# Kernel tuning notes

Measured on AMD Instinct MI355X. Metric: run time of the kernel, lower is better.

The kernel has to match this reference:

```python
import jax, jax.numpy as jnp
import numpy as np

B_CHUNK = 5          # hardcoded self.B in the module
GAMMA = 0.9865
BATCH, SEQ, FEAT, DIM = 8, 4000, 256, 256


def setup_inputs() -> dict:
    key = jax.random.key(0)
    ks = jax.random.split(key, 6)
    xq = jax.random.normal(ks[0], (BATCH, SEQ, FEAT), jnp.float32)
    xk = jax.random.normal(ks[1], (BATCH, SEQ, FEAT), jnp.float32)
    xv = jax.random.normal(ks[2], (BATCH, SEQ, FEAT), jnp.float32)
    scale = 1.0 / np.sqrt(FEAT).astype(np.float32)
    Wq = jax.random.normal(ks[3], (FEAT, DIM), jnp.float32) * scale
    Wk = jax.random.normal(ks[4], (FEAT, DIM), jnp.float32) * scale
    Wv = jax.random.normal(ks[5], (FEAT, DIM), jnp.float32) * scale
    return {"xq": xq, "xk": xk, "xv": xv, "Wq": Wq, "Wk": Wk, "Wv": Wv}


def reference(xq, xk, xv, Wq, Wk, Wv):
    gamma = jnp.float32(GAMMA)
    B = B_CHUNK
    b, seq, _ = xq.shape
    dim = Wq.shape[1]
    n = seq // B  # number of chunks

    # projections, chunked: [b, n, B, dim]
    Q = (xq @ Wq).reshape(b, n, B, dim)
    K = (xk @ Wk).reshape(b, n, B, dim)
    V = (xv @ Wv).reshape(b, n, B, dim)

    chunk_idx = jnp.arange(n, dtype=jnp.float32)
    # Z[i] = gamma^(B - i - 1) (per-chunk scalar, as in original)
    Z = gamma ** (jnp.float32(B) - chunk_idx - 1.0)
    Vz = V * Z[None, :, None, None]

    # intra-chunk decay matrix: L[i,j] = gamma^(j-i) for i >= j, else 0
    pos = jnp.arange(B, dtype=jnp.float32)
    L = jnp.tril(gamma ** (pos[None, :] - pos[:, None]))

    # intra-chunk term: (Q K^T * L) @ V, vectorized over all chunks
    S = jnp.einsum('bnid,bnjd->bnij', Q, K)          # [b, n, B, B]
    intra = jnp.einsum('bnij,bnjd->bnid', S * L, V)  # [b, n, B, dim]

    # cross-chunk recurrence: R[i] = K_i^T Vz_i + gamma^B R[i-1]
    # X[i-1] += Q_i @ R[i-1] * gamma^(i+1)
    Qn = jnp.moveaxis(Q, 1, 0)   # [n, b, B, dim]
    Kn = jnp.moveaxis(K, 1, 0)
    Vzn = jnp.moveaxis(Vz, 1, 0)
    gB = gamma ** B

    def step(R_prev, inp):
        qi, ki, vzi, i = inp
        cross_prev = jnp.einsum('bod,bde->boe', qi, R_prev) * gamma ** (i + 1.0)
        R_new = jnp.einsum('bod,boe->bde', ki, vzi) + gB * R_prev
        return R_new, cross_prev

    R0 = jnp.zeros((b, dim, dim), xq.dtype)
    _, ys = jax.lax.scan(step, R0, (Qn, Kn, Vzn, chunk_idx))  # ys[i] = cross for chunk i-1
    cross = jnp.concatenate([ys[1:], jnp.zeros_like(ys[:1])], axis=0)  # last chunk has no cross term
    cross = jnp.moveaxis(cross, 0, 1)  # [b, n, B, dim]

    X = intra + cross
    return X.reshape(b, seq, dim)
```

## Files before the change

kernel.cpp:

```cpp
#include <hip/hip_runtime.h>
#include <cmath>

#define GAMMA 0.9865f
#define L2G   -0.01960905f
#define BATCH 8
#define SEQ   4000
#define CSUP  25
#define GSUP  32
#define RPG   125

typedef _Float16 half8 __attribute__((ext_vector_type(8)));
typedef _Float16 half4 __attribute__((ext_vector_type(4)));
typedef float    floatx4 __attribute__((ext_vector_type(4)));

__device__ __forceinline__ float gpow(float e) { return exp2f(e * L2G); }

__global__ __launch_bounds__(256) void wt_convert(
    const float* __restrict__ Wq, const float* __restrict__ Wk, const float* __restrict__ Wv,
    _Float16* __restrict__ Wt) {
    int t = blockIdx.x * 256 + threadIdx.x;
    int mat = t >> 16, rem = t & 65535;
    int n = rem >> 8, k = rem & 255;
    const float* W = (mat == 0) ? Wq : (mat == 1) ? Wk : Wv;
    Wt[(size_t)mat * 65536 + n * 256 + k] = (_Float16)W[k * 256 + n];
}

__global__ __launch_bounds__(256, 2) void qkv_gemm_f16(
    const float* __restrict__ xq, const float* __restrict__ xk, const float* __restrict__ xv,
    const _Float16* __restrict__ WtAll,
    _Float16* __restrict__ Qb, _Float16* __restrict__ Kb, _Float16* __restrict__ Vb) {
    int op = blockIdx.y;
    const float* x = (op == 0) ? xq : (op == 1) ? xk : xv;
    const _Float16* Wt = WtAll + (size_t)op * 65536;
    _Float16* dst = (op == 0) ? Qb : (op == 1) ? Kb : Vb;

    __shared__ _Float16 Xs[128][40];
    __shared__ _Float16 WsT[256][40];

    int t = threadIdx.x;
    int lane = t & 63, wave = t >> 6;
    int ln = lane & 15, q8 = (lane >> 4) << 3, q4 = (lane >> 4) << 2;
    int row0 = blockIdx.x * 128;

    floatx4 acc[8][4] = {};

    for (int dt = 0; dt < 8; ++dt) {
        int k0 = dt * 32;
#pragma unroll
        for (int i = 0; i < 4; ++i) {
            int idx = t + i * 256;
            int m = idx >> 3, kk = (idx & 7) << 2;
            floatx4 v = *(const floatx4*)&x[(size_t)(row0 + m) * 256 + k0 + kk];
            half4 h; h[0] = (_Float16)v[0]; h[1] = (_Float16)v[1];
            h[2] = (_Float16)v[2]; h[3] = (_Float16)v[3];
            *(half4*)&Xs[m][kk] = h;
        }
#pragma unroll
        for (int i = 0; i < 4; ++i) {
            int idx = t + i * 256;
            int n = idx >> 2, kk = (idx & 3) << 3;
            *(half8*)&WsT[n][kk] = *(const half8*)&Wt[n * 256 + k0 + kk];
        }
        __syncthreads();
        half8 af[8];
#pragma unroll
        for (int mi = 0; mi < 8; ++mi) af[mi] = *(const half8*)&Xs[mi * 16 + ln][q8];
#pragma unroll
        for (int ni = 0; ni < 4; ++ni) {
            half8 bf = *(const half8*)&WsT[(wave * 4 + ni) * 16 + ln][q8];
#pragma unroll
            for (int mi = 0; mi < 8; ++mi)
                acc[mi][ni] = __builtin_amdgcn_mfma_f32_16x16x32_f16(af[mi], bf, acc[mi][ni], 0, 0, 0);
        }
        __syncthreads();
    }
#pragma unroll
    for (int mi = 0; mi < 8; ++mi)
#pragma unroll
        for (int ni = 0; ni < 4; ++ni)
#pragma unroll
            for (int r = 0; r < 4; ++r) {
                int row = row0 + mi * 16 + q4 + r;
                int col = (wave * 4 + ni) * 16 + ln;
                dst[(size_t)row * 256 + col] = (_Float16)acc[mi][ni][r];
            }
}

__global__ __launch_bounds__(256, 2) void chunk_states_mfma(
    const _Float16* __restrict__ Kb, const _Float16* __restrict__ Vb,
    _Float16* __restrict__ Wh) {
    int eh = blockIdx.x, g = blockIdx.y, b = blockIdx.z;
    int t = threadIdx.x, lane = t & 63, wave = t >> 6;
    int ln = lane & 15, q8 = (lane >> 4) << 3, q4 = (lane >> 4) << 2;
    __shared__ __align__(16) _Float16 Vs[32 * 136];
    __shared__ __align__(16) _Float16 Ks[32 * 264];
    size_t base_row = (size_t)b * SEQ + g * RPG;
    floatx4 acc[8][4] = {};
    for (int kt = 0; kt < 4; ++kt) {
        int r0 = kt * 32;
#pragma unroll
        for (int i = 0; i < 2; ++i) {
            int idx = t + i * 256;
            int r = idx >> 4, e8 = (idx & 15) << 3;
            half8 v = {};
            if (r0 + r < RPG) {
                v = *(const half8*)&Vb[(base_row + r0 + r) * 256 + eh * 128 + e8];
                int mloc = (r0 + r) / 5;
                float a = gpow((float)(149 - 6 * mloc));
#pragma unroll
                for (int z = 0; z < 8; ++z) v[z] = (_Float16)((float)v[z] * a);
            }
            *(half8*)&Vs[r * 136 + e8] = v;
        }
#pragma unroll
        for (int i = 0; i < 4; ++i) {
            int idx = t + i * 256;
            int r = idx >> 5, d8 = (idx & 31) << 3;
            half8 v = {};
            if (r0 + r < RPG) v = *(const half8*)&Kb[(base_row + r0 + r) * 256 + d8];
            *(half8*)&Ks[r * 264 + d8] = v;
        }
        __syncthreads();
        half8 Af[8], Bf[4];
#pragma unroll
        for (int mi = 0; mi < 8; ++mi)
#pragma unroll
            for (int j = 0; j < 8; ++j) Af[mi][j] = Vs[(q8 + j) * 136 + mi * 16 + ln];
#pragma unroll
        for (int ni = 0; ni < 4; ++ni)
#pragma unroll
            for (int j = 0; j < 8; ++j) Bf[ni][j] = Ks[(q8 + j) * 264 + wave * 64 + ni * 16 + ln];
#pragma unroll
        for (int mi = 0; mi < 8; ++mi)
#pragma unroll
            for (int ni = 0; ni < 4; ++ni)
                acc[mi][ni] = __builtin_amdgcn_mfma_f32_16x16x32_f16(Af[mi], Bf[ni], acc[mi][ni], 0, 0, 0);
        __syncthreads();
    }
    size_t ob = ((size_t)(g * 8 + b)) << 16;
#pragma unroll
    for (int mi = 0; mi < 8; ++mi)
#pragma unroll
        for (int ni = 0; ni < 4; ++ni)
#pragma unroll
            for (int r = 0; r < 4; ++r) {
                int e = eh * 128 + mi * 16 + q4 + r;
                int d = wave * 64 + ni * 16 + ln;
                Wh[ob + (size_t)e * 256 + d] = (_Float16)acc[mi][ni][r];
            }
}

__global__ __launch_bounds__(256) void state_scan(
    const _Float16* __restrict__ Wh, _Float16* __restrict__ SprevT) {
    int t = blockIdx.x * 256 + threadIdx.x;
    int b = t >> 13;
    int idx = (t & 8191) << 3;
    const float gF = gpow(150.0f);
    float s[8] = {};
    for (int g = 0; g < GSUP; ++g) {
        size_t o = (((size_t)(g * 8 + b)) << 16) + idx;
        half8 w = *(const half8*)&Wh[o];
        half8 sv;
#pragma unroll
        for (int z = 0; z < 8; ++z) { sv[z] = (_Float16)s[z]; s[z] = (float)w[z] + gF * s[z]; }
        *(half8*)&SprevT[o] = sv;
    }
}

__global__ __launch_bounds__(256) void intra_sc(
    const _Float16* __restrict__ Qb, const _Float16* __restrict__ Kb, float* __restrict__ scw) {
    int b = blockIdx.y;
    int j = blockIdx.x * 4 + (threadIdx.x >> 6);
    int lane = threadIdx.x & 63;
    size_t base = ((size_t)b * SEQ + j * 5) * 256 + lane * 4;
    half4 qv[5], kv[5];
#pragma unroll
    for (int p = 0; p < 5; ++p) {
        qv[p] = *(const half4*)&Qb[base + p * 256];
        kv[p] = *(const half4*)&Kb[base + p * 256];
    }
#pragma unroll
    for (int p = 0; p < 5; ++p)
#pragma unroll
        for (int q = 0; q <= p; ++q) {
            float s = 0.f;
#pragma unroll
            for (int z = 0; z < 4; ++z) s += (float)qv[p][z] * (float)kv[q][z];
#pragma unroll
            for (int off = 32; off; off >>= 1) s += __shfl_xor(s, off, 64);
            if (lane == 0) scw[((size_t)b * 800 + j) * 25 + p * 5 + q] = s * gpow((float)(q - p));
        }
}

__global__ __launch_bounds__(256, 2) void cross_f16(
    const _Float16* __restrict__ Qb, const _Float16* __restrict__ Kb,
    const _Float16* __restrict__ Vb, const _Float16* __restrict__ SprevT,
    const float* __restrict__ scw, float* __restrict__ out) {
    int eq = blockIdx.x, g = blockIdx.y, b = blockIdx.z;
    int e0 = eq * 64;
    int t = threadIdx.x;
    int lane = t & 63, wave = t >> 6;
    int ln = lane & 15, q8 = (lane >> 4) << 3, q4 = (lane >> 4) << 2;
    int m4 = (wave >> 1) * 4;
    int c4 = (wave & 1) * 4;
    int e2 = (wave & 1) * 2;

    __shared__ __align__(16) char smem[60416];
    _Float16* QsB  = (_Float16*)smem;
    _Float16* KsB  = (_Float16*)(smem + 10240);
    _Float16* VsTB = (_Float16*)smem;
    _Float16* SsB  = (_Float16*)(smem + 20480);
    _Float16* PsB  = (_Float16*)(smem + 25600);
#define QS(m_, k_)  QsB[(m_) * 40 + (k_)]
#define KS(m_, k_)  KsB[(m_) * 40 + (k_)]
#define SS(m_, k_)  SsB[(m_) * 40 + (k_)]
#define PS(m_, k_)  PsB[(m_) * 136 + (k_)]
#define VST(m_, k_) VsTB[(m_) * 136 + (k_)]

    size_t kvbase = (size_t)b * SEQ + g * RPG;
    size_t sb = ((size_t)(g * 8 + b)) << 16;

    floatx4 pacc[4][4] = {};
    floatx4 acc[4][2] = {};

    for (int dt = 0; dt < 8; ++dt) {
        int d0 = dt * 32;
#pragma unroll
        for (int i = 0; i < 2; ++i) {
            int idx = t + i * 256;
            int m = idx >> 2, kk = (idx & 3) << 3;
            int qr = g * RPG + 5 + m;
            half8 v = {};
            if (m < 125 && qr < SEQ) v = *(const half8*)&Qb[((size_t)b * SEQ + qr) * 256 + d0 + kk];
            *(half8*)&QS(m, kk) = v;
        }
#pragma unroll
        for (int i = 0; i < 2; ++i) {
            int idx = t + i * 256;
            int cp = idx >> 2, kk = (idx & 3) << 3;
            half8 v = {};
            if (cp < 125) v = *(const half8*)&Kb[(kvbase + cp) * 256 + d0 + kk];
            *(half8*)&KS(cp, kk) = v;
        }
        {
            int ee = t >> 2, kk = (t & 3) << 3;
            *(half8*)&SS(ee, kk) = *(const half8*)&SprevT[sb + (size_t)(e0 + ee) * 256 + d0 + kk];
        }
        __syncthreads();
        half8 af[4];
#pragma unroll
        for (int mi = 0; mi < 4; ++mi) af[mi] = *(const half8*)&QS((m4 + mi) * 16 + ln, q8);
#pragma unroll
        for (int ci = 0; ci < 4; ++ci) {
            half8 bf = *(const half8*)&KS((c4 + ci) * 16 + ln, q8);
#pragma unroll
            for (int mi = 0; mi < 4; ++mi)
                pacc[mi][ci] = __builtin_amdgcn_mfma_f32_16x16x32_f16(af[mi], bf, pacc[mi][ci], 0, 0, 0);
        }
#pragma unroll
        for (int ei = 0; ei < 2; ++ei) {
            half8 bf = *(const half8*)&SS((e2 + ei) * 16 + ln, q8);
#pragma unroll
            for (int mi = 0; mi < 4; ++mi)
                acc[mi][ei] = __builtin_amdgcn_mfma_f32_16x16x32_f16(af[mi], bf, acc[mi][ei], 0, 0, 0);
        }
        __syncthreads();
    }

#pragma unroll
    for (int mi = 0; mi < 4; ++mi)
#pragma unroll
        for (int r = 0; r < 4; ++r) {
            int rp = (m4 + mi) * 16 + q4 + r;
            int rc = rp / 5;
            float rs = 0.f;
            if (rp < 125 && !(g == GSUP - 1 && rc == CSUP - 1)) rs = gpow((float)(6 * rc + 7));
            acc[mi][0][r] *= rs;
            acc[mi][1][r] *= rs;
        }

#pragma unroll
    for (int i = 0; i < 32; ++i) {
        int idx = t + i * 256;
        int cp = idx >> 6, ee = idx & 63;
        _Float16 v = (_Float16)0.f;
        if (cp < 125) v = Vb[(kvbase + cp) * 256 + e0 + ee];
        VST(ee, cp) = v;
    }
#pragma unroll
    for (int mi = 0; mi < 4; ++mi)
#pragma unroll
        for (int ci = 0; ci < 4; ++ci)
#pragma unroll
            for (int r = 0; r < 4; ++r) {
                int rp = (m4 + mi) * 16 + q4 + r;
                int cp = (c4 + ci) * 16 + ln;
                int rc = rp / 5, cc = cp / 5;
                float w = 0.f;
                if (rp < 125 && cp < 125 && cc <= rc && !(g == GSUP - 1 && rc == CSUP - 1))
                    w = gpow((float)(6 * (rc - cc + 1)));
                PS(rp, cp) = (_Float16)(pacc[mi][ci][r] * w);
            }
    __syncthreads();

#pragma unroll
    for (int ct = 0; ct < 4; ++ct) {
        int cp0 = ct * 32;
        half8 paf[4];
#pragma unroll
        for (int mi = 0; mi < 4; ++mi) paf[mi] = *(const half8*)&PS((m4 + mi) * 16 + ln, cp0 + q8);
#pragma unroll
        for (int ei = 0; ei < 2; ++ei) {
            half8 bv = *(const half8*)&VST((e2 + ei) * 16 + ln, cp0 + q8);
#pragma unroll
            for (int mi = 0; mi < 4; ++mi)
                acc[mi][ei] = __builtin_amdgcn_mfma_f32_16x16x32_f16(paf[mi], bv, acc[mi][ei], 0, 0, 0);
        }
    }

#pragma unroll
    for (int mi = 0; mi < 4; ++mi)
#pragma unroll
        for (int r = 0; r < 4; ++r) {
            int rp = (m4 + mi) * 16 + q4 + r;
            if (rp < 125) {
                int rc = rp / 5, pp = rp - rc * 5;
                const float* srow = scw + ((size_t)b * 800 + g * 25 + rc) * 25 + pp * 5;
                float a0 = acc[mi][0][r], a1 = acc[mi][1][r];
                for (int q = 0; q <= pp; ++q) {
                    float s = srow[q];
                    a0 += s * (float)VST(e2 * 16 + ln, rc * 5 + q);
                    a1 += s * (float)VST((e2 + 1) * 16 + ln, rc * 5 + q);
                }
                size_t orow = ((size_t)b * SEQ + g * RPG + rp) * 256;
                out[orow + e0 + e2 * 16 + ln] = a0;
                out[orow + e0 + (e2 + 1) * 16 + ln] = a1;
            }
        }
}

extern "C" void kernel_launch(void* const* d_in, const int* in_sizes, int n_in,
                              void* d_out, int out_size, void* d_ws, size_t ws_size,
                              hipStream_t stream) {
    const float* xq = (const float*)d_in[0];
    const float* xk = (const float*)d_in[1];
    const float* xv = (const float*)d_in[2];
    const float* Wq = (const float*)d_in[3];
    const float* Wk = (const float*)d_in[4];
    const float* Wv = (const float*)d_in[5];
    float* out = (float*)d_out;

    const size_t NELEM = (size_t)SEQ * BATCH * 256;
    _Float16* Qb = (_Float16*)d_ws;
    _Float16* Kb = Qb + NELEM;
    _Float16* Vb = Kb + NELEM;
    _Float16* Wt = Vb + NELEM;
    _Float16* Wh = Wt + 196608;
    _Float16* SprevT = Wh + (size_t)GSUP * BATCH * 65536;
    float* scw = (float*)(SprevT + (size_t)GSUP * BATCH * 65536);

    wt_convert<<<dim3(768), 256, 0, stream>>>(Wq, Wk, Wv, Wt);
    qkv_gemm_f16<<<dim3(250, 3), 256, 0, stream>>>(xq, xk, xv, Wt, Qb, Kb, Vb);
    chunk_states_mfma<<<dim3(2, 32, 8), 256, 0, stream>>>(Kb, Vb, Wh);
    state_scan<<<dim3(256), 256, 0, stream>>>(Wh, SprevT);
    intra_sc<<<dim3(200, 8), 256, 0, stream>>>(Qb, Kb, scw);
    cross_f16<<<dim3(4, 32, 8), 256, 0, stream>>>(Qb, Kb, Vb, SprevT, scw, out);
}
```

Before: 274.9 us.

## Double-buffer GEMM and cross kernels; pre-transpose V into a separate kernel

Adds register-prefetched double buffering to the QKV projection GEMM and to the cross kernel, so global loads for the next K-tile overlap MFMA work and one barrier per iteration is removed. A new vt_transpose kernel writes V in a transposed, chunk-grouped layout. The cross kernel can then load V with vector half8 reads instead of scalar strided gathers. VT reuses the Wh workspace after state_scan has consumed it. The cost is an extra kernel launch and more shared memory and registers, which may lower occupancy.

```diff
diff --git a/kernel.cpp b/kernel.cpp
--- a/kernel.cpp
+++ b/kernel.cpp
@@ -34,45 +34,57 @@
     const _Float16* Wt = WtAll + (size_t)op * 65536;
     _Float16* dst = (op == 0) ? Qb : (op == 1) ? Kb : Vb;
 
-    __shared__ _Float16 Xs[128][40];
-    __shared__ _Float16 WsT[256][40];
+    __shared__ _Float16 Xs[2][128][40];
+    __shared__ _Float16 WsT[2][256][40];
 
     int t = threadIdx.x;
     int lane = t & 63, wave = t >> 6;
     int ln = lane & 15, q8 = (lane >> 4) << 3, q4 = (lane >> 4) << 2;
     int row0 = blockIdx.x * 128;
 
+    int xm = t >> 3, xk_ = (t & 7) << 2;
+    int wr = t >> 2, wk = (t & 3) << 3;
+
     floatx4 acc[8][4] = {};
-
+    floatx4 xn[4]; half8 wn[4];
+
+    auto loadNext = [&](int dt) {
+        int k0 = dt * 32;
+#pragma unroll
+        for (int i = 0; i < 4; ++i)
+            xn[i] = *(const floatx4*)&x[(size_t)(row0 + xm + i * 32) * 256 + k0 + xk_];
+#pragma unroll
+        for (int i = 0; i < 4; ++i)
+            wn[i] = *(const half8*)&Wt[(wr + i * 64) * 256 + k0 + wk];
+    };
+    auto writeBuf = [&](int bf) {
+#pragma unroll
+        for (int i = 0; i < 4; ++i) {
+            half4 h; h[0] = (_Float16)xn[i][0]; h[1] = (_Float16)xn[i][1];
+            h[2] = (_Float16)xn[i][2]; h[3] = (_Float16)xn[i][3];
+            *(half4*)&Xs[bf][xm + i * 32][xk_] = h;
+        }
+#pragma unroll
+        for (int i = 0; i < 4; ++i)
+            *(half8*)&WsT[bf][wr + i * 64][wk] = wn[i];
+    };
+
+    loadNext(0); writeBuf(0);
+    int cur = 0;
     for (int dt = 0; dt < 8; ++dt) {
-        int k0 = dt * 32;
-#pragma unroll
-        for (int i = 0; i < 4; ++i) {
-            int idx = t + i * 256;
-            int m = idx >> 3, kk = (idx & 7) << 2;
-            floatx4 v = *(const floatx4*)&x[(size_t)(row0 + m) * 256 + k0 + kk];
-            half4 h; h[0] = (_Float16)v[0]; h[1] = (_Float16)v[1];
-            h[2] = (_Float16)v[2]; h[3] = (_Float16)v[3];
-            *(half4*)&Xs[m][kk] = h;
-        }
-#pragma unroll
-        for (int i = 0; i < 4; ++i) {
-            int idx = t + i * 256;
-            int n = idx >> 2, kk = (idx & 3) << 3;
-            *(half8*)&WsT[n][kk] = *(const half8*)&Wt[n * 256 + k0 + kk];
-        }
         __syncthreads();
+        if (dt < 7) loadNext(dt + 1);
         half8 af[8];
 #pragma unroll
-        for (int mi = 0; mi < 8; ++mi) af[mi] = *(const half8*)&Xs[mi * 16 + ln][q8];
+        for (int mi = 0; mi < 8; ++mi) af[mi] = *(const half8*)&Xs[cur][mi * 16 + ln][q8];
 #pragma unroll
         for (int ni = 0; ni < 4; ++ni) {
-            half8 bf = *(const half8*)&WsT[(wave * 4 + ni) * 16 + ln][q8];
+            half8 bf = *(const half8*)&WsT[cur][(wave * 4 + ni) * 16 + ln][q8];
 #pragma unroll
             for (int mi = 0; mi < 8; ++mi)
                 acc[mi][ni] = __builtin_amdgcn_mfma_f32_16x16x32_f16(af[mi], bf, acc[mi][ni], 0, 0, 0);
         }
-        __syncthreads();
+        if (dt < 7) { writeBuf(cur ^ 1); cur ^= 1; }
     }
 #pragma unroll
     for (int mi = 0; mi < 8; ++mi)
@@ -84,6 +96,35 @@
                 int col = (wave * 4 + ni) * 16 + ln;
                 dst[(size_t)row * 256 + col] = (_Float16)acc[mi][ni][r];
             }
+}
+
+__global__ __launch_bounds__(256) void vt_transpose(
+    const _Float16* __restrict__ Vb, _Float16* __restrict__ VT) {
+    int es = blockIdx.x, g = blockIdx.y, b = blockIdx.z;
+    int t = threadIdx.x;
+    __shared__ __align__(16) _Float16 Ls[64 * 136];
+#pragma unroll
+    for (int i = 0; i < 4; ++i) {
+        int idx = t + i * 256;
+        int cp = idx >> 3, eg = idx & 7;
+        half8 v = {};
+        if (cp < 125)
+            v = *(const half8*)&Vb[((size_t)b * SEQ + g * RPG + cp) * 256 + es * 64 + eg * 8];
+        int cpg = cp >> 3, c7 = cp & 7;
+#pragma unroll
+        for (int z = 0; z < 8; ++z) {
+            int e = eg * 8 + z;
+            Ls[e * 136 + ((cpg ^ (e >> 3)) << 3) + c7] = v[z];
+        }
+    }
+    __syncthreads();
+#pragma unroll
+    for (int jj = 0; jj < 4; ++jj) {
+        int ee = jj * 16 + (t >> 4);
+        int cpg = t & 15;
+        half8 h = *(const half8*)&Ls[ee * 136 + ((cpg ^ (ee >> 3)) << 3)];
+        *(half8*)&VT[(((size_t)b * 256 + es * 64 + ee) * 32 + g) * 128 + cpg * 8] = h;
+    }
 }
 
 __global__ __launch_bounds__(256, 2) void chunk_states_mfma(
@@ -194,7 +235,7 @@
 
 __global__ __launch_bounds__(256, 2) void cross_f16(
     const _Float16* __restrict__ Qb, const _Float16* __restrict__ Kb,
-    const _Float16* __restrict__ Vb, const _Float16* __restrict__ SprevT,
+    const _Float16* __restrict__ VT, const _Float16* __restrict__ SprevT,
     const float* __restrict__ scw, float* __restrict__ out) {
     int eq = blockIdx.x, g = blockIdx.y, b = blockIdx.z;
     int e0 = eq * 64;
@@ -205,66 +246,81 @@
     int c4 = (wave & 1) * 4;
     int e2 = (wave & 1) * 2;
 
-    __shared__ __align__(16) char smem[60416];
+    __shared__ __align__(16) char smem[52224];
     _Float16* QsB  = (_Float16*)smem;
-    _Float16* KsB  = (_Float16*)(smem + 10240);
+    _Float16* KsB  = (_Float16*)(smem + 20480);
+    _Float16* SsB  = (_Float16*)(smem + 40960);
     _Float16* VsTB = (_Float16*)smem;
-    _Float16* SsB  = (_Float16*)(smem + 20480);
-    _Float16* PsB  = (_Float16*)(smem + 25600);
-#define QS(m_, k_)  QsB[(m_) * 40 + (k_)]
-#define KS(m_, k_)  KsB[(m_) * 40 + (k_)]
-#define SS(m_, k_)  SsB[(m_) * 40 + (k_)]
+    _Float16* PsB  = (_Float16*)(smem + 17408);
+#define QS(bf_, m_, k_)  QsB[(bf_) * 5120 + (m_) * 40 + (k_)]
+#define KS(bf_, m_, k_)  KsB[(bf_) * 5120 + (m_) * 40 + (k_)]
+#define SS(bf_, m_, k_)  SsB[(bf_) * 2560 + (m_) * 40 + (k_)]
 #define PS(m_, k_)  PsB[(m_) * 136 + (k_)]
 #define VST(m_, k_) VsTB[(m_) * 136 + (k_)]
 
     size_t kvbase = (size_t)b * SEQ + g * RPG;
     size_t sb = ((size_t)(g * 8 + b)) << 16;
 
+    int sm = t >> 2, skk = (t & 3) << 3;
+
     floatx4 pacc[4][4] = {};
     floatx4 acc[4][2] = {};
-
+    half8 qn[2], kn[2], sn;
+    half8 vtp[4];
+
+    auto loadNext = [&](int dt) {
+        int d0 = dt * 32;
+        half8 z = {};
+#pragma unroll
+        for (int i = 0; i < 2; ++i) {
+            int m = sm + i * 64;
+            int qr = g * RPG + 5 + m;
+            qn[i] = z;
+            if (m < 125 && qr < SEQ) qn[i] = *(const half8*)&Qb[((size_t)b * SEQ + qr) * 256 + d0 + skk];
+            kn[i] = z;
+            if (m < 125) kn[i] = *(const half8*)&Kb[(kvbase + m) * 256 + d0 + skk];
+        }
+        sn = *(const half8*)&SprevT[sb + (size_t)(e0 + sm) * 256 + d0 + skk];
+    };
+    auto writeBuf = [&](int bf) {
+#pragma unroll
+        for (int i = 0; i < 2; ++i) {
+            int m = sm + i * 64;
+            *(half8*)&QS(bf, m, skk) = qn[i];
+            *(half8*)&KS(bf, m, skk) = kn[i];
+        }
+        *(half8*)&SS(bf, sm, skk) = sn;
+    };
+
+    loadNext(0); writeBuf(0);
+    int cur = 0;
     for (int dt = 0; dt < 8; ++dt) {
-        int d0 = dt * 32;
-#pragma unroll
-        for (int i = 0; i < 2; ++i) {
-            int idx = t + i * 256;
-            int m = idx >> 2, kk = (idx & 3) << 3;
-            int qr = g * RPG + 5 + m;
-            half8 v = {};
-            if (m < 125 && qr < SEQ) v = *(const half8*)&Qb[((size_t)b * SEQ + qr) * 256 + d0 + kk];
-            *(half8*)&QS(m, kk) = v;
-        }
-#pragma unroll
-        for (int i = 0; i < 2; ++i) {
-            int idx = t + i * 256;
-            int cp = idx >> 2, kk = (idx & 3) << 3;
-            half8 v = {};
-            if (cp < 125) v = *(const half8*)&Kb[(kvbase + cp) * 256 + d0 + kk];
-            *(half8*)&KS(cp, kk) = v;
-        }
-        {
-            int ee = t >> 2, kk = (t & 3) << 3;
-            *(half8*)&SS(ee, kk) = *(const half8*)&SprevT[sb + (size_t)(e0 + ee) * 256 + d0 + kk];
-        }
         __syncthreads();
+        if (dt < 7) loadNext(dt + 1);
+        if (dt == 7) {
+            size_t vtbase = (((size_t)b * 256 + e0 + sm) * 32 + g) * 128;
+#pragma unroll
+            for (int j = 0; j < 4; ++j)
+                vtp[j] = *(const half8*)&VT[vtbase + ((j * 4 + (t & 3)) << 3)];
+        }
         half8 af[4];
 #pragma unroll
-        for (int mi = 0; mi < 4; ++mi) af[mi] = *(const half8*)&QS((m4 + mi) * 16 + ln, q8);
+        for (int mi = 0; mi < 4; ++mi) af[mi] = *(const half8*)&QS(cur, (m4 + mi) * 16 + ln, q8);
 #pragma unroll
         for (int ci = 0; ci < 4; ++ci) {
-            half8 bf = *(const half8*)&KS((c4 + ci) * 16 + ln, q8);
+            half8 bf = *(const half8*)&KS(cur, (c4 + ci) * 16 + ln, q8);
 #pragma unroll
             for (int mi = 0; mi < 4; ++mi)
                 pacc[mi][ci] = __builtin_amdgcn_mfma_f32_16x16x32_f16(af[mi], bf, pacc[mi][ci], 0, 0, 0);
         }
 #pragma unroll
         for (int ei = 0; ei < 2; ++ei) {
-            half8 bf = *(const half8*)&SS((e2 + ei) * 16 + ln, q8);
+            half8 bf = *(const half8*)&SS(cur, (e2 + ei) * 16 + ln, q8);
 #pragma unroll
             for (int mi = 0; mi < 4; ++mi)
                 acc[mi][ei] = __builtin_amdgcn_mfma_f32_16x16x32_f16(af[mi], bf, acc[mi][ei], 0, 0, 0);
         }
-        __syncthreads();
+        if (dt < 7) { writeBuf(cur ^ 1); cur ^= 1; }
     }
 
 #pragma unroll
@@ -279,13 +335,13 @@
             acc[mi][1][r] *= rs;
         }
 
-#pragma unroll
-    for (int i = 0; i < 32; ++i) {
-        int idx = t + i * 256;
-        int cp = idx >> 6, ee = idx & 63;
-        _Float16 v = (_Float16)0.f;
-        if (cp < 125) v = Vb[(kvbase + cp) * 256 + e0 + ee];
-        VST(ee, cp) = v;
+    __syncthreads();
+
+    {
+        int sg = t & 3;
+#pragma unroll
+        for (int j = 0; j < 4; ++j)
+            *(half8*)&VST(sm, (j * 4 + sg) << 3) = vtp[j];
     }
 #pragma unroll
     for (int mi = 0; mi < 4; ++mi)
@@ -358,11 +414,13 @@
     _Float16* Wh = Wt + 196608;
     _Float16* SprevT = Wh + (size_t)GSUP * BATCH * 65536;
     float* scw = (float*)(SprevT + (size_t)GSUP * BATCH * 65536);
+    _Float16* VT = Wh;
 
     wt_convert<<<dim3(768), 256, 0, stream>>>(Wq, Wk, Wv, Wt);
     qkv_gemm_f16<<<dim3(250, 3), 256, 0, stream>>>(xq, xk, xv, Wt, Qb, Kb, Vb);
     chunk_states_mfma<<<dim3(2, 32, 8), 256, 0, stream>>>(Kb, Vb, Wh);
     state_scan<<<dim3(256), 256, 0, stream>>>(Wh, SprevT);
+    vt_transpose<<<dim3(4, 32, 8), 256, 0, stream>>>(Vb, VT);
     intra_sc<<<dim3(200, 8), 256, 0, stream>>>(Qb, Kb, scw);
-    cross_f16<<<dim3(4, 32, 8), 256, 0, stream>>>(Qb, Kb, Vb, SprevT, scw, out);
-}
+    cross_f16<<<dim3(4, 32, 8), 256, 0, stream>>>(Qb, Kb, VT, SprevT, scw, out);
+}
```

Measured after the change: 269.1 us. 2.1% less time.
